# Kernel optimization log

Measured on AMD Instinct MI355X. Metric: run time of the kernel, lower is better.

Reference implementation:

```python
import jax, jax.numpy as jnp
import numpy as np


def _conv(x, w):
    # 'same'-padded NCHW conv, stride 1, no bias (matches nn.Conv2d(..., padding=k//2, bias=False))
    return jax.lax.conv_general_dilated(x, w, (1, 1), 'SAME',
                                        dimension_numbers=('NCHW', 'OIHW', 'NCHW'))


def setup_inputs() -> dict:
    key = jax.random.key(0)
    ks = jax.random.split(key, 11)
    b, C, H, W = 8, 64, 192, 192
    n_classes, n_space = 2, 8
    return {
        'x': jax.random.normal(ks[0], (b, C, H, W), jnp.float32),
        'class_score': jax.random.normal(ks[1], (b, n_classes, H, W), jnp.float32),
        # to_cspace: Conv2d(1, n_space-1, 3, padding=1)
        'W_cspace': jax.random.normal(ks[2], (n_space - 1, 1, 3, 3), jnp.float32) * 0.1,
        # to_xspace: Conv2d(C, C*n_space, 3, padding=1)
        'W_xspace': jax.random.normal(ks[3], (C * n_space, C, 3, 3), jnp.float32) * 0.02,
        # 1x1 convs stored as squeezed vectors (no bias)
        'W_combine_space': jax.random.normal(ks[4], (n_space,), jnp.float32) * 0.3,  # Conv2d(n_space,1,1)
        'W_cvalue': jax.random.normal(ks[5], (n_space,), jnp.float32) * 0.3,        # Conv2d(1,n_space,1)
        'W_attn': jax.random.normal(ks[6], (n_space,), jnp.float32) * 0.3,          # Conv2d(1,n_space,1)
        'W_combine': jax.random.normal(ks[7], (n_space,), jnp.float32) * 0.3,       # Conv2d(n_space,1,1)
        # single_conv: Conv2d(C,C,3) + BatchNorm2d(C) + ReLU
        'W_single': jax.random.normal(ks[8], (C, C, 3, 3), jnp.float32) * 0.02,
        'bn_gamma': jnp.ones((C,), jnp.float32),
        'bn_beta': jnp.zeros((C,), jnp.float32),
    }


def reference(x, class_score, W_cspace, W_xspace, W_combine_space, W_cvalue,
              W_attn, W_combine, W_single, bn_gamma, bn_beta):
    b, C, H, Wd = x.shape
    nc = class_score.shape[1]           # n_classes
    s = W_cvalue.shape[0]               # n_space
    class_prob = jax.nn.sigmoid(class_score)                       # (b, c, H, W)

    # per-class spatial 'spaces'
    space0 = class_prob.reshape(b * nc, 1, H, Wd)                  # (b*c, 1, H, W)
    space = jnp.concatenate([space0, jax.nn.sigmoid(_conv(space0, W_cspace))], axis=1)  # (b*c, s, H, W)
    space_norm = space / jnp.sum(space, axis=(2, 3), keepdims=True)
    space_norm = space_norm.reshape(b, nc, s, H, Wd).transpose(0, 2, 1, 3, 4)  # (b, s, c, H, W)

    # project x into s spaces, then contract over spatial dims (replaces broadcast-mul + double sum)
    xv = _conv(x, W_xspace).reshape(b, s, C, H, Wd)                # (b, s, d, H, W)
    tok = jnp.einsum('bsdhw,bschw->bscd', xv, space_norm)          # (b, s, c, d)
    tok = jnp.einsum('s,bscd->bcd', W_combine_space, tok)          # combine_space 1x1 conv -> (b, c, d)

    # class value / attention (1x1 convs over a singleton channel == broadcast scale)
    cval = tok[:, None] * W_cvalue[None, :, None, None]            # (b, s, c, d)
    attn = class_prob.reshape(b, nc, H * Wd).transpose(0, 2, 1)    # (b, hw, c)
    attn = jax.nn.sigmoid(attn[:, None] * W_attn[None, :, None, None])  # (b, s, hw, c)

    # attention matmul + combine 1x1 conv fused into one contraction (linear ops commute)
    info = jnp.einsum('s,bsnc,bscd->bnd', W_combine, attn, cval)   # (b, hw, d)
    info = info.transpose(0, 2, 1).reshape(b, C, H, Wd)            # (b, d, H, W)

    # single_conv: conv3x3 -> BatchNorm2d (training-mode batch stats, biased var) -> ReLU
    y = _conv(info, W_single)
    mean = jnp.mean(y, axis=(0, 2, 3), keepdims=True)
    var = jnp.var(y, axis=(0, 2, 3), keepdims=True)
    y = jax.nn.relu((y - mean) * jax.lax.rsqrt(var + 1e-5)
                    * bn_gamma[None, :, None, None] + bn_beta[None, :, None, None])
    return x + y
```

## Files before the change

kernel.cpp:

```cpp
#include <hip/hip_runtime.h>
#include <math.h>

#define B   8
#define C   64
#define HH  192
#define WWD 192
#define P   (HH*WWD)
#define NC  2
#define NS  8
#define PP  (194*194)

#define OFF_SPACE 0
#define OFF_WT    0
#define OFF_GM    294912
#define OFF_SPART 4817408
#define OFF_R     4835840
#define OFF_TOK2  4909568
#define OFF_U     4910592
#define OFF_STP   4919808
#define OFF_SCALE 4956672
#define OFF_SHIFT 4956736
#define WS_FLOATS 4956800

__device__ __forceinline__ float sigm(float x) { return 1.0f / (1.0f + expf(-x)); }

__global__ void k_space(const float* __restrict__ cs, const float* __restrict__ Wc,
                        float* __restrict__ spp, float* __restrict__ Spart) {
    int m = blockIdx.y;
    int bx = blockIdx.x;
    int p = bx * 256 + threadIdx.x;
    int h = p / WWD, w = p - (p / WWD) * WWD;
    float cp[9];
    #pragma unroll
    for (int ky = 0; ky < 3; ky++)
        #pragma unroll
        for (int kx = 0; kx < 3; kx++) {
            int hh = h + ky - 1, ww = w + kx - 1;
            float v = 0.f;
            if ((unsigned)hh < HH && (unsigned)ww < WWD)
                v = sigm(cs[m * P + hh * WWD + ww]);
            cp[ky * 3 + kx] = v;
        }
    float ch[8];
    ch[0] = cp[4];
    #pragma unroll
    for (int j = 0; j < 7; j++) {
        float a = 0.f;
        #pragma unroll
        for (int k = 0; k < 9; k++) a += Wc[j * 9 + k] * cp[k];
        ch[j + 1] = sigm(a);
    }
    #pragma unroll
    for (int q = 0; q < 8; q++)
        spp[(m * 8 + q) * PP + (h + 1) * 194 + (w + 1)] = ch[q];
    __shared__ float red[4][8];
    int lane = threadIdx.x & 63, wave = threadIdx.x >> 6;
    #pragma unroll
    for (int q = 0; q < 8; q++) {
        float v = ch[q];
        for (int off = 32; off > 0; off >>= 1) v += __shfl_down(v, off);
        if (lane == 0) red[wave][q] = v;
    }
    __syncthreads();
    if (threadIdx.x < 8) {
        int q = threadIdx.x;
        Spart[(m * 8 + q) * 144 + bx] = red[0][q] + red[1][q] + red[2][q] + red[3][q];
    }
}

__launch_bounds__(256, 3)
__global__ void k_R2(const float* __restrict__ x, const float* __restrict__ spp,
                     float* __restrict__ R) {
    int ig = blockIdx.x;
    int scz = blockIdx.y;
    int b  = blockIdx.z;
    int sc = scz & 15;
    int half = scz >> 4;
    int s = sc >> 1, c = sc & 1;
    const float* xb = x + (b * C + ig * 8) * P;
    const float* sp = spp + ((b * NC + c) * NS + s) * PP;

    float acc[8][9];
    #pragma unroll
    for (int i = 0; i < 8; i++)
        #pragma unroll
        for (int t = 0; t < 9; t++) acc[i][t] = 0.f;

    for (int it = half * 18; it < half * 18 + 18; it++) {
        int p0 = it * 1024 + threadIdx.x * 4;
        int h = p0 / WWD, w0 = p0 - (p0 / WWD) * WWD;
        float4 xv[8];
        #pragma unroll
        for (int i = 0; i < 8; i++) xv[i] = *(const float4*)(xb + i * P + p0);
        float g[3][6];
        #pragma unroll
        for (int ty = 0; ty < 3; ty++) {
            const float* rp = sp + (h + 2 - ty) * 194 + w0;
            float4 ga; float2 gb;
            __builtin_memcpy(&ga, rp, 16);
            __builtin_memcpy(&gb, rp + 4, 8);
            g[ty][0] = ga.x; g[ty][1] = ga.y; g[ty][2] = ga.z;
            g[ty][3] = ga.w; g[ty][4] = gb.x; g[ty][5] = gb.y;
        }
        #pragma unroll
        for (int ty = 0; ty < 3; ty++)
            #pragma unroll
            for (int tx = 0; tx < 3; tx++) {
                float g0 = g[ty][2 - tx], g1 = g[ty][3 - tx];
                float g2 = g[ty][4 - tx], g3 = g[ty][5 - tx];
                #pragma unroll
                for (int i = 0; i < 8; i++) {
                    float a = acc[i][ty * 3 + tx];
                    a += xv[i].x * g0; a += xv[i].y * g1;
                    a += xv[i].z * g2; a += xv[i].w * g3;
                    acc[i][ty * 3 + tx] = a;
                }
            }
    }

    __shared__ float red[4][72];
    int lane = threadIdx.x & 63, wave = threadIdx.x >> 6;
    #pragma unroll
    for (int i = 0; i < 8; i++)
        #pragma unroll
        for (int t = 0; t < 9; t++) {
            float v = acc[i][t];
            for (int off = 32; off > 0; off >>= 1) v += __shfl_down(v, off);
            if (lane == 0) red[wave][i * 9 + t] = v;
        }
    __syncthreads();
    if (threadIdx.x < 72) {
        int i = threadIdx.x / 9, t = threadIdx.x - (threadIdx.x / 9) * 9;
        float v = red[0][threadIdx.x] + red[1][threadIdx.x] +
                  red[2][threadIdx.x] + red[3][threadIdx.x];
        atomicAdd(&R[((b * 16 + sc) * 64 + (ig * 8 + i)) * 9 + t], v);
    }
}

__global__ void k_wt(const float* __restrict__ Wxs, float* __restrict__ Wt) {
    int t = blockIdx.x;
    int s = blockIdx.y;
    int d = threadIdx.x;
    Wt[(s * 576 + t) * 64 + d] = Wxs[(s * 64 + d) * 576 + t];
}

__global__ void k_g(const float* __restrict__ cs, const float* __restrict__ Wcval,
                    const float* __restrict__ Wattn, const float* __restrict__ Wcomb,
                    float* __restrict__ gmap) {
    int m = blockIdx.y;
    int p = blockIdx.x * 256 + threadIdx.x;
    float wa[8], wt[8];
    #pragma unroll
    for (int s = 0; s < 8; s++) { wa[s] = Wcomb[s] * Wcval[s]; wt[s] = Wattn[s]; }
    float cp = sigm(cs[m * P + p]);
    float a = 0.f;
    #pragma unroll
    for (int s = 0; s < 8; s++) a += wa[s] * sigm(cp * wt[s]);
    gmap[m * P + p] = a;
}

__global__ void k_tok2(const float* __restrict__ Wt, const float* __restrict__ Wcs,
                       const float* __restrict__ R, const float* __restrict__ Spart,
                       float* __restrict__ tok2) {
    int bc = blockIdx.x, s = blockIdx.y;
    int d = threadIdx.x;
    const float* spp = Spart + (bc * 8 + s) * 144;
    float sv = 0.f;
    for (int k = d; k < 144; k += 64) sv += spp[k];
    #pragma unroll
    for (int msk = 32; msk >= 1; msk >>= 1) sv += __shfl_xor(sv, msk);

    const float* Rp = R + ((bc & 1) + ((bc >> 1) * 16 + s * 2)) * 576;
    const float* Wp = Wt + s * 576 * 64 + d;
    float a = 0.f;
    #pragma unroll 4
    for (int t = 0; t < 576; t++) a += Wp[t * 64] * Rp[t];
    float val = a * Wcs[s] / sv;
    atomicAdd(&tok2[bc * C + d], val);
}

__global__ void k_U(const float* __restrict__ Ws, const float* __restrict__ tok2,
                    float* __restrict__ U) {
    int b = blockIdx.x, m = blockIdx.y, oc = threadIdx.x;
    const float* tp = tok2 + (b * NC + m) * C;
    float u[9];
    #pragma unroll
    for (int t = 0; t < 9; t++) u[t] = 0.f;
    for (int ci = 0; ci < C; ci++) {
        float tv = tp[ci];
        const float* wp = Ws + (oc * C + ci) * 9;
        #pragma unroll
        for (int t = 0; t < 9; t++) u[t] += wp[t] * tv;
    }
    float* up = U + ((b * C + oc) * 2 + m) * 9;
    #pragma unroll
    for (int t = 0; t < 9; t++) up[t] = u[t];
}

__device__ __forceinline__ void stage_g(const float* __restrict__ gmap, int b, int ty0, int tx0,
                                        float* h0, float* h1) {
    const float* g0p = gmap + (b * NC + 0) * P;
    const float* g1p = gmap + (b * NC + 1) * P;
    for (int idx = threadIdx.x; idx < 34 * 34; idx += 256) {
        int i = idx / 34, j = idx - (idx / 34) * 34;
        int gy = ty0 - 1 + i, gx = tx0 - 1 + j;
        float a0 = 0.f, a1 = 0.f;
        if ((unsigned)gy < HH && (unsigned)gx < WWD) {
            int p = gy * WWD + gx;
            a0 = g0p[p]; a1 = g1p[p];
        }
        h0[i * 35 + j] = a0; h1[i * 35 + j] = a1;
    }
}

__launch_bounds__(256)
__global__ void k_cs(const float* __restrict__ gmap, const float* __restrict__ U,
                     float* __restrict__ STp) {
    int tile = blockIdx.x, ocg = blockIdx.y, b = blockIdx.z;
    int ty0 = (tile / 6) * 32, tx0 = (tile % 6) * 32;
    __shared__ float h0[34 * 35], h1[34 * 35];
    stage_g(gmap, b, ty0, tx0, h0, h1);
    __syncthreads();

    int w = __builtin_amdgcn_readfirstlane(threadIdx.x >> 6);
    int lane = threadIdx.x & 63;
    int oc0 = ocg * 8 + w * 2;
    float u0[2][9], u1[2][9];
    #pragma unroll
    for (int j = 0; j < 2; j++) {
        const float* up = U + ((b * C + oc0 + j) * 2) * 9;
        #pragma unroll
        for (int t = 0; t < 9; t++) { u0[j][t] = up[t]; u1[j][t] = up[9 + t]; }
    }
    float s1[2] = {0.f, 0.f}, s2[2] = {0.f, 0.f};
    for (int it = 0; it < 4; it++) {
        int row = it * 8 + (lane >> 3);
        int c0 = (lane & 7) * 4;
        float g0v[3][6], g1v[3][6];
        #pragma unroll
        for (int dy = 0; dy < 3; dy++)
            #pragma unroll
            for (int dx = 0; dx < 6; dx++) {
                g0v[dy][dx] = h0[(row + dy) * 35 + c0 + dx];
                g1v[dy][dx] = h1[(row + dy) * 35 + c0 + dx];
            }
        #pragma unroll
        for (int j = 0; j < 2; j++)
            #pragma unroll
            for (int px = 0; px < 4; px++) {
                float y = 0.f;
                #pragma unroll
                for (int ky = 0; ky < 3; ky++)
                    #pragma unroll
                    for (int kx = 0; kx < 3; kx++) {
                        y += u0[j][ky * 3 + kx] * g0v[ky][px + kx];
                        y += u1[j][ky * 3 + kx] * g1v[ky][px + kx];
                    }
                s1[j] += y; s2[j] += y * y;
            }
    }
    #pragma unroll
    for (int j = 0; j < 2; j++) {
        float a = s1[j], q = s2[j];
        for (int off = 32; off > 0; off >>= 1) { a += __shfl_down(a, off); q += __shfl_down(q, off); }
        if (lane == 0) {
            int slot = b * 36 + tile;
            STp[slot * 64 + (oc0 + j)] = a;
            STp[288 * 64 + slot * 64 + (oc0 + j)] = q;
        }
    }
}

__global__ void k_bnfin(const float* __restrict__ STp, const float* __restrict__ gamma,
                        const float* __restrict__ beta, float* __restrict__ scale,
                        float* __restrict__ shift) {
    int oc = threadIdx.x;
    double s = 0.0, s2 = 0.0;
    for (int k = 0; k < 288; k++) {
        s  += (double)STp[k * 64 + oc];
        s2 += (double)STp[288 * 64 + k * 64 + oc];
    }
    double n = (double)(B * P);
    double mean = s / n;
    double var = s2 / n - mean * mean;
    float sc = gamma[oc] * rsqrtf((float)var + 1e-5f);
    scale[oc] = sc;
    shift[oc] = beta[oc] - (float)mean * sc;
}

__launch_bounds__(256)
__global__ void k_fin2(const float* __restrict__ gmap, const float* __restrict__ U,
                       const float* __restrict__ x,
                       const float* __restrict__ scale, const float* __restrict__ shift,
                       float* __restrict__ out) {
    int tile = blockIdx.x, ocg = blockIdx.y, b = blockIdx.z;
    int ty0 = (tile / 6) * 32, tx0 = (tile % 6) * 32;
    __shared__ float h0[34 * 35], h1[34 * 35];
    stage_g(gmap, b, ty0, tx0, h0, h1);
    __syncthreads();

    int w = __builtin_amdgcn_readfirstlane(threadIdx.x >> 6);
    int lane = threadIdx.x & 63;
    int oc0 = ocg * 8 + w * 2;
    float u0[2][9], u1[2][9], sc[2], sh[2];
    #pragma unroll
    for (int j = 0; j < 2; j++) {
        const float* up = U + ((b * C + oc0 + j) * 2) * 9;
        #pragma unroll
        for (int t = 0; t < 9; t++) { u0[j][t] = up[t]; u1[j][t] = up[9 + t]; }
        sc[j] = scale[oc0 + j]; sh[j] = shift[oc0 + j];
    }
    for (int it = 0; it < 4; it++) {
        int row = it * 8 + (lane >> 3);
        int c0 = (lane & 7) * 4;
        float g0v[3][6], g1v[3][6];
        #pragma unroll
        for (int dy = 0; dy < 3; dy++)
            #pragma unroll
            for (int dx = 0; dx < 6; dx++) {
                g0v[dy][dx] = h0[(row + dy) * 35 + c0 + dx];
                g1v[dy][dx] = h1[(row + dy) * 35 + c0 + dx];
            }
        #pragma unroll
        for (int j = 0; j < 2; j++) {
            float y4[4];
            #pragma unroll
            for (int px = 0; px < 4; px++) {
                float y = 0.f;
                #pragma unroll
                for (int ky = 0; ky < 3; ky++)
                    #pragma unroll
                    for (int kx = 0; kx < 3; kx++) {
                        y += u0[j][ky * 3 + kx] * g0v[ky][px + kx];
                        y += u1[j][ky * 3 + kx] * g1v[ky][px + kx];
                    }
                y4[px] = y;
            }
            int ga = (b * C + oc0 + j) * P + (ty0 + row) * WWD + tx0 + c0;
            float4 xv = *(const float4*)(x + ga);
            float4 ov;
            ov.x = fmaxf(y4[0] * sc[j] + sh[j], 0.f) + xv.x;
            ov.y = fmaxf(y4[1] * sc[j] + sh[j], 0.f) + xv.y;
            ov.z = fmaxf(y4[2] * sc[j] + sh[j], 0.f) + xv.z;
            ov.w = fmaxf(y4[3] * sc[j] + sh[j], 0.f) + xv.w;
            *(float4*)(out + ga) = ov;
        }
    }
}

extern "C" void kernel_launch(void* const* d_in, const int* in_sizes, int n_in,
                              void* d_out, int out_size, void* d_ws, size_t ws_size,
                              hipStream_t stream) {
    const float* x     = (const float*)d_in[0];
    const float* cs    = (const float*)d_in[1];
    const float* Wc    = (const float*)d_in[2];
    const float* Wxs   = (const float*)d_in[3];
    const float* Wcsp  = (const float*)d_in[4];
    const float* Wcval = (const float*)d_in[5];
    const float* Wattn = (const float*)d_in[6];
    const float* Wcomb = (const float*)d_in[7];
    const float* Wsing = (const float*)d_in[8];
    const float* gamma = (const float*)d_in[9];
    const float* beta  = (const float*)d_in[10];
    float* ws  = (float*)d_ws;
    float* out = (float*)d_out;

    float* spp   = ws + OFF_SPACE;
    float* Wt    = ws + OFF_WT;
    float* gmap  = ws + OFF_GM;
    float* Spart = ws + OFF_SPART;
    float* R     = ws + OFF_R;
    float* tok2  = ws + OFF_TOK2;
    float* U     = ws + OFF_U;
    float* STp   = ws + OFF_STP;
    float* scale = ws + OFF_SCALE;
    float* shift = ws + OFF_SHIFT;

    hipMemsetAsync(ws, 0, (size_t)(OFF_TOK2 + 1024) * sizeof(float), stream);

    k_space<<<dim3(144, 16), 256, 0, stream>>>(cs, Wc, spp, Spart);
    k_R2   <<<dim3(8, 32, 8), 256, 0, stream>>>(x, spp, R);
    k_wt   <<<dim3(576, 8), 64, 0, stream>>>(Wxs, Wt);
    k_g    <<<dim3(144, 16), 256, 0, stream>>>(cs, Wcval, Wattn, Wcomb, gmap);
    k_tok2 <<<dim3(16, 8), 64, 0, stream>>>(Wt, Wcsp, R, Spart, tok2);
    k_U    <<<dim3(8, 2), 64, 0, stream>>>(Wsing, tok2, U);
    k_cs   <<<dim3(36, 8, 8), 256, 0, stream>>>(gmap, U, STp);
    k_bnfin<<<1, 64, 0, stream>>>(STp, gamma, beta, scale, shift);
    k_fin2 <<<dim3(36, 8, 8), 256, 0, stream>>>(gmap, U, x, scale, shift, out);
}
```

Before: 426.6 us.

## Rebalance small kernels and reuse staged tiles across output-channel groups

```diff
diff --git a/kernel.cpp b/kernel.cpp
--- a/kernel.cpp
+++ b/kernel.cpp
@@ -13,6 +13,7 @@
 #define OFF_SPACE 0
 #define OFF_WT    0
 #define OFF_GM    294912
+#define OFF_WST   884736
 #define OFF_SPART 4817408
 #define OFF_R     4835840
 #define OFF_TOK2  4909568
@@ -137,11 +138,20 @@
     }
 }
 
-__global__ void k_wt(const float* __restrict__ Wxs, float* __restrict__ Wt) {
-    int t = blockIdx.x;
-    int s = blockIdx.y;
-    int d = threadIdx.x;
-    Wt[(s * 576 + t) * 64 + d] = Wxs[(s * 64 + d) * 576 + t];
+__global__ void k_wtb(const float* __restrict__ Wxs, const float* __restrict__ Ws,
+                      float* __restrict__ Wt, float* __restrict__ WsT) {
+    int blk = blockIdx.x;
+    if (blk < 1152) {
+        int o = blk * 256 + threadIdx.x;
+        int d = o & 63, r = o >> 6;
+        int s = r / 576, t = r - s * 576;
+        Wt[o] = Wxs[(s * 64 + d) * 576 + t];
+    } else {
+        int o = (blk - 1152) * 256 + threadIdx.x;
+        int ci = o / 576, q = o - ci * 576;
+        int t = q >> 6, oc = q & 63;
+        WsT[o] = Ws[(oc * 64 + ci) * 9 + t];
+    }
 }
 
 __global__ void k_g(const float* __restrict__ cs, const float* __restrict__ Wcval,
@@ -162,7 +172,7 @@
 __global__ void k_tok2(const float* __restrict__ Wt, const float* __restrict__ Wcs,
                        const float* __restrict__ R, const float* __restrict__ Spart,
                        float* __restrict__ tok2) {
-    int bc = blockIdx.x, s = blockIdx.y;
+    int bc = blockIdx.x, s = blockIdx.y, tz = blockIdx.z;
     int d = threadIdx.x;
     const float* spp = Spart + (bc * 8 + s) * 144;
     float sv = 0.f;
@@ -173,28 +183,25 @@
     const float* Rp = R + ((bc & 1) + ((bc >> 1) * 16 + s * 2)) * 576;
     const float* Wp = Wt + s * 576 * 64 + d;
     float a = 0.f;
-    #pragma unroll 4
-    for (int t = 0; t < 576; t++) a += Wp[t * 64] * Rp[t];
+    int t0 = tz * 144;
+    #pragma unroll 8
+    for (int t = t0; t < t0 + 144; t++) a += Wp[t * 64] * Rp[t];
     float val = a * Wcs[s] / sv;
     atomicAdd(&tok2[bc * C + d], val);
 }
 
-__global__ void k_U(const float* __restrict__ Ws, const float* __restrict__ tok2,
+__global__ void k_U(const float* __restrict__ WsT, const float* __restrict__ tok2,
                     float* __restrict__ U) {
-    int b = blockIdx.x, m = blockIdx.y, oc = threadIdx.x;
-    const float* tp = tok2 + (b * NC + m) * C;
-    float u[9];
-    #pragma unroll
-    for (int t = 0; t < 9; t++) u[t] = 0.f;
-    for (int ci = 0; ci < C; ci++) {
-        float tv = tp[ci];
-        const float* wp = Ws + (oc * C + ci) * 9;
-        #pragma unroll
-        for (int t = 0; t < 9; t++) u[t] += wp[t] * tv;
-    }
-    float* up = U + ((b * C + oc) * 2 + m) * 9;
-    #pragma unroll
-    for (int t = 0; t < 9; t++) up[t] = u[t];
+    int b = blockIdx.x, m = blockIdx.y;
+    int tid = threadIdx.x;
+    int oc = tid & 63, t = tid >> 6;
+    __shared__ float tok[64];
+    if (tid < 64) tok[tid] = tok2[(b * NC + m) * C + tid];
+    __syncthreads();
+    float a = 0.f;
+    #pragma unroll 8
+    for (int ci = 0; ci < C; ci++) a += WsT[ci * 576 + tid] * tok[ci];
+    U[((b * C + oc) * 2 + m) * 9 + t] = a;
 }
 
 __device__ __forceinline__ void stage_g(const float* __restrict__ gmap, int b, int ty0, int tx0,
@@ -216,7 +223,7 @@
 __launch_bounds__(256)
 __global__ void k_cs(const float* __restrict__ gmap, const float* __restrict__ U,
                      float* __restrict__ STp) {
-    int tile = blockIdx.x, ocg = blockIdx.y, b = blockIdx.z;
+    int tile = blockIdx.x, og2 = blockIdx.y, b = blockIdx.z;
     int ty0 = (tile / 6) * 32, tx0 = (tile % 6) * 32;
     __shared__ float h0[34 * 35], h1[34 * 35];
     stage_g(gmap, b, ty0, tx0, h0, h1);
@@ -224,49 +231,51 @@
 
     int w = __builtin_amdgcn_readfirstlane(threadIdx.x >> 6);
     int lane = threadIdx.x & 63;
-    int oc0 = ocg * 8 + w * 2;
-    float u0[2][9], u1[2][9];
-    #pragma unroll
-    for (int j = 0; j < 2; j++) {
-        const float* up = U + ((b * C + oc0 + j) * 2) * 9;
-        #pragma unroll
-        for (int t = 0; t < 9; t++) { u0[j][t] = up[t]; u1[j][t] = up[9 + t]; }
-    }
-    float s1[2] = {0.f, 0.f}, s2[2] = {0.f, 0.f};
-    for (int it = 0; it < 4; it++) {
-        int row = it * 8 + (lane >> 3);
-        int c0 = (lane & 7) * 4;
-        float g0v[3][6], g1v[3][6];
-        #pragma unroll
-        for (int dy = 0; dy < 3; dy++)
-            #pragma unroll
-            for (int dx = 0; dx < 6; dx++) {
-                g0v[dy][dx] = h0[(row + dy) * 35 + c0 + dx];
-                g1v[dy][dx] = h1[(row + dy) * 35 + c0 + dx];
+    for (int g4 = 0; g4 < 4; g4++) {
+        int oc0 = (og2 * 4 + g4) * 8 + w * 2;
+        float u0[2][9], u1[2][9];
+        #pragma unroll
+        for (int j = 0; j < 2; j++) {
+            const float* up = U + ((b * C + oc0 + j) * 2) * 9;
+            #pragma unroll
+            for (int t = 0; t < 9; t++) { u0[j][t] = up[t]; u1[j][t] = up[9 + t]; }
+        }
+        float s1[2] = {0.f, 0.f}, s2[2] = {0.f, 0.f};
+        for (int it = 0; it < 4; it++) {
+            int row = it * 8 + (lane >> 3);
+            int c0 = (lane & 7) * 4;
+            float g0v[3][6], g1v[3][6];
+            #pragma unroll
+            for (int dy = 0; dy < 3; dy++)
+                #pragma unroll
+                for (int dx = 0; dx < 6; dx++) {
+                    g0v[dy][dx] = h0[(row + dy) * 35 + c0 + dx];
+                    g1v[dy][dx] = h1[(row + dy) * 35 + c0 + dx];
+                }
+            #pragma unroll
+            for (int j = 0; j < 2; j++)
+                #pragma unroll
+                for (int px = 0; px < 4; px++) {
+                    float y = 0.f;
+                    #pragma unroll
+                    for (int ky = 0; ky < 3; ky++)
+                        #pragma unroll
+                        for (int kx = 0; kx < 3; kx++) {
+                            y += u0[j][ky * 3 + kx] * g0v[ky][px + kx];
+                            y += u1[j][ky * 3 + kx] * g1v[ky][px + kx];
+                        }
+                    s1[j] += y; s2[j] += y * y;
+                }
+        }
+        #pragma unroll
+        for (int j = 0; j < 2; j++) {
+            float a = s1[j], q = s2[j];
+            for (int off = 32; off > 0; off >>= 1) { a += __shfl_down(a, off); q += __shfl_down(q, off); }
+            if (lane == 0) {
+                int slot = b * 36 + tile;
+                STp[slot * 64 + (oc0 + j)] = a;
+                STp[288 * 64 + slot * 64 + (oc0 + j)] = q;
             }
-        #pragma unroll
-        for (int j = 0; j < 2; j++)
-            #pragma unroll
-            for (int px = 0; px < 4; px++) {
-                float y = 0.f;
-                #pragma unroll
-                for (int ky = 0; ky < 3; ky++)
-                    #pragma unroll
-                    for (int kx = 0; kx < 3; kx++) {
-                        y += u0[j][ky * 3 + kx] * g0v[ky][px + kx];
-                        y += u1[j][ky * 3 + kx] * g1v[ky][px + kx];
-                    }
-                s1[j] += y; s2[j] += y * y;
-            }
-    }
-    #pragma unroll
-    for (int j = 0; j < 2; j++) {
-        float a = s1[j], q = s2[j];
-        for (int off = 32; off > 0; off >>= 1) { a += __shfl_down(a, off); q += __shfl_down(q, off); }
-        if (lane == 0) {
-            int slot = b * 36 + tile;
-            STp[slot * 64 + (oc0 + j)] = a;
-            STp[288 * 64 + slot * 64 + (oc0 + j)] = q;
         }
     }
 }
@@ -274,18 +283,25 @@
 __global__ void k_bnfin(const float* __restrict__ STp, const float* __restrict__ gamma,
                         const float* __restrict__ beta, float* __restrict__ scale,
                         float* __restrict__ shift) {
-    int oc = threadIdx.x;
+    int oc = threadIdx.x & 63, q = threadIdx.x >> 6;
     double s = 0.0, s2 = 0.0;
-    for (int k = 0; k < 288; k++) {
+    for (int k = q * 72; k < q * 72 + 72; k++) {
         s  += (double)STp[k * 64 + oc];
         s2 += (double)STp[288 * 64 + k * 64 + oc];
     }
-    double n = (double)(B * P);
-    double mean = s / n;
-    double var = s2 / n - mean * mean;
-    float sc = gamma[oc] * rsqrtf((float)var + 1e-5f);
-    scale[oc] = sc;
-    shift[oc] = beta[oc] - (float)mean * sc;
+    __shared__ double ls[4][64], ls2[4][64];
+    ls[q][oc] = s; ls2[q][oc] = s2;
+    __syncthreads();
+    if (threadIdx.x < 64) {
+        double S  = ls[0][oc] + ls[1][oc] + ls[2][oc] + ls[3][oc];
+        double S2 = ls2[0][oc] + ls2[1][oc] + ls2[2][oc] + ls2[3][oc];
+        double n = (double)(B * P);
+        double mean = S / n;
+        double var = S2 / n - mean * mean;
+        float sc = gamma[oc] * rsqrtf((float)var + 1e-5f);
+        scale[oc] = sc;
+        shift[oc] = beta[oc] - (float)mean * sc;
+    }
 }
 
 __launch_bounds__(256)
@@ -293,7 +309,7 @@
                        const float* __restrict__ x,
                        const float* __restrict__ scale, const float* __restrict__ shift,
                        float* __restrict__ out) {
-    int tile = blockIdx.x, ocg = blockIdx.y, b = blockIdx.z;
+    int tile = blockIdx.x, og2 = blockIdx.y, b = blockIdx.z;
     int ty0 = (tile / 6) * 32, tx0 = (tile % 6) * 32;
     __shared__ float h0[34 * 35], h1[34 * 35];
     stage_g(gmap, b, ty0, tx0, h0, h1);
@@ -301,49 +317,51 @@
 
     int w = __builtin_amdgcn_readfirstlane(threadIdx.x >> 6);
     int lane = threadIdx.x & 63;
-    int oc0 = ocg * 8 + w * 2;
-    float u0[2][9], u1[2][9], sc[2], sh[2];
-    #pragma unroll
-    for (int j = 0; j < 2; j++) {
-        const float* up = U + ((b * C + oc0 + j) * 2) * 9;
-        #pragma unroll
-        for (int t = 0; t < 9; t++) { u0[j][t] = up[t]; u1[j][t] = up[9 + t]; }
-        sc[j] = scale[oc0 + j]; sh[j] = shift[oc0 + j];
-    }
-    for (int it = 0; it < 4; it++) {
-        int row = it * 8 + (lane >> 3);
-        int c0 = (lane & 7) * 4;
-        float g0v[3][6], g1v[3][6];
-        #pragma unroll
-        for (int dy = 0; dy < 3; dy++)
-            #pragma unroll
-            for (int dx = 0; dx < 6; dx++) {
-                g0v[dy][dx] = h0[(row + dy) * 35 + c0 + dx];
-                g1v[dy][dx] = h1[(row + dy) * 35 + c0 + dx];
+    for (int g4 = 0; g4 < 4; g4++) {
+        int oc0 = (og2 * 4 + g4) * 8 + w * 2;
+        float u0[2][9], u1[2][9], sc[2], sh[2];
+        #pragma unroll
+        for (int j = 0; j < 2; j++) {
+            const float* up = U + ((b * C + oc0 + j) * 2) * 9;
+            #pragma unroll
+            for (int t = 0; t < 9; t++) { u0[j][t] = up[t]; u1[j][t] = up[9 + t]; }
+            sc[j] = scale[oc0 + j]; sh[j] = shift[oc0 + j];
+        }
+        for (int it = 0; it < 4; it++) {
+            int row = it * 8 + (lane >> 3);
+            int c0 = (lane & 7) * 4;
+            float g0v[3][6], g1v[3][6];
+            #pragma unroll
+            for (int dy = 0; dy < 3; dy++)
+                #pragma unroll
+                for (int dx = 0; dx < 6; dx++) {
+                    g0v[dy][dx] = h0[(row + dy) * 35 + c0 + dx];
+                    g1v[dy][dx] = h1[(row + dy) * 35 + c0 + dx];
+                }
+            #pragma unroll
+            for (int j = 0; j < 2; j++) {
+                float y4[4];
+                #pragma unroll
+                for (int px = 0; px < 4; px++) {
+                    float y = 0.f;
+                    #pragma unroll
+                    for (int ky = 0; ky < 3; ky++)
+                        #pragma unroll
+                        for (int kx = 0; kx < 3; kx++) {
+                            y += u0[j][ky * 3 + kx] * g0v[ky][px + kx];
+                            y += u1[j][ky * 3 + kx] * g1v[ky][px + kx];
+                        }
+                    y4[px] = y;
+                }
+                int ga = (b * C + oc0 + j) * P + (ty0 + row) * WWD + tx0 + c0;
+                float4 xv = *(const float4*)(x + ga);
+                float4 ov;
+                ov.x = fmaxf(y4[0] * sc[j] + sh[j], 0.f) + xv.x;
+                ov.y = fmaxf(y4[1] * sc[j] + sh[j], 0.f) + xv.y;
+                ov.z = fmaxf(y4[2] * sc[j] + sh[j], 0.f) + xv.z;
+                ov.w = fmaxf(y4[3] * sc[j] + sh[j], 0.f) + xv.w;
+                *(float4*)(out + ga) = ov;
             }
-        #pragma unroll
-        for (int j = 0; j < 2; j++) {
-            float y4[4];
-            #pragma unroll
-            for (int px = 0; px < 4; px++) {
-                float y = 0.f;
-                #pragma unroll
-                for (int ky = 0; ky < 3; ky++)
-                    #pragma unroll
-                    for (int kx = 0; kx < 3; kx++) {
-                        y += u0[j][ky * 3 + kx] * g0v[ky][px + kx];
-                        y += u1[j][ky * 3 + kx] * g1v[ky][px + kx];
-                    }
-                y4[px] = y;
-            }
-            int ga = (b * C + oc0 + j) * P + (ty0 + row) * WWD + tx0 + c0;
-            float4 xv = *(const float4*)(x + ga);
-            float4 ov;
-            ov.x = fmaxf(y4[0] * sc[j] + sh[j], 0.f) + xv.x;
-            ov.y = fmaxf(y4[1] * sc[j] + sh[j], 0.f) + xv.y;
-            ov.z = fmaxf(y4[2] * sc[j] + sh[j], 0.f) + xv.z;
-            ov.w = fmaxf(y4[3] * sc[j] + sh[j], 0.f) + xv.w;
-            *(float4*)(out + ga) = ov;
         }
     }
 }
@@ -368,6 +386,7 @@
     float* spp   = ws + OFF_SPACE;
     float* Wt    = ws + OFF_WT;
     float* gmap  = ws + OFF_GM;
+    float* WsT   = ws + OFF_WST;
     float* Spart = ws + OFF_SPART;
     float* R     = ws + OFF_R;
     float* tok2  = ws + OFF_TOK2;
@@ -380,11 +399,11 @@
 
     k_space<<<dim3(144, 16), 256, 0, stream>>>(cs, Wc, spp, Spart);
     k_R2   <<<dim3(8, 32, 8), 256, 0, stream>>>(x, spp, R);
-    k_wt   <<<dim3(576, 8), 64, 0, stream>>>(Wxs, Wt);
+    k_wtb  <<<dim3(1296), 256, 0, stream>>>(Wxs, Wsing, Wt, WsT);
     k_g    <<<dim3(144, 16), 256, 0, stream>>>(cs, Wcval, Wattn, Wcomb, gmap);
-    k_tok2 <<<dim3(16, 8), 64, 0, stream>>>(Wt, Wcsp, R, Spart, tok2);
-    k_U    <<<dim3(8, 2), 64, 0, stream>>>(Wsing, tok2, U);
-    k_cs   <<<dim3(36, 8, 8), 256, 0, stream>>>(gmap, U, STp);
-    k_bnfin<<<1, 64, 0, stream>>>(STp, gamma, beta, scale, shift);
-    k_fin2 <<<dim3(36, 8, 8), 256, 0, stream>>>(gmap, U, x, scale, shift, out);
-}
+    k_tok2 <<<dim3(16, 8, 4), 64, 0, stream>>>(Wt, Wcsp, R, Spart, tok2);
+    k_U    <<<dim3(8, 2), 576, 0, stream>>>(WsT, tok2, U);
+    k_cs   <<<dim3(36, 2, 8), 256, 0, stream>>>(gmap, U, STp);
+    k_bnfin<<<1, 256, 0, stream>>>(STp, gamma, beta, scale, shift);
+    k_fin2 <<<dim3(36, 2, 8), 256, 0, stream>>>(gmap, U, x, scale, shift, out);
+}
```

New measurement: 380.2 us. 1.12x faster.
